# Performance work log

Measured on AMD Instinct MI355X. Metric: run time of the kernel, lower is better.

## Reference

```python
import jax, jax.numpy as jnp
import numpy as np

NUM_V = 500_000      # num (k-1)-simplices (vertices)
NUM_E = 1_500_000    # num k-simplices (edges)
NNZ = 2 * NUM_E      # 2 oriented incidences per edge
D_FEAT = 64


def setup_inputs() -> dict:
    key = jax.random.key(0)
    k1, k2, k3, k4 = jax.random.split(key, 4)
    simplex_features = jax.random.normal(k1, (NUM_E, D_FEAT), dtype=jnp.float32)
    # oriented incidence values are +/-1
    boundary_values = jnp.sign(jax.random.normal(k2, (NNZ,), dtype=jnp.float32))
    boundary_values = jnp.where(boundary_values == 0, 1.0, boundary_values)
    boundary_rows = jax.random.randint(k3, (NNZ,), 0, NUM_V, dtype=jnp.int32)
    boundary_cols = jax.random.randint(k4, (NNZ,), 0, NUM_E, dtype=jnp.int32)
    return {
        "simplex_features": simplex_features,
        "boundary_values": boundary_values,
        "boundary_rows": boundary_rows,
        "boundary_cols": boundary_cols,
        "num_out": NUM_V,
    }


def reference(simplex_features, boundary_values, boundary_rows, boundary_cols, num_out):
    # SpMM: out[r, :] += val * features[c, :] over all nonzeros (r, c, val).
    gathered = boundary_values[:, None] * simplex_features[boundary_cols]  # [nnz, d]
    out = jax.ops.segment_sum(gathered, boundary_rows, num_segments=num_out)  # [num_out, d]
    return out
```

## Files before the change

### kernel.cpp

```cpp
#include <hip/hip_runtime.h>

#define D_FEAT 64
#define SCAN_BLOCK 256
#define SCAN_ITEMS 16
#define SCAN_CHUNK (SCAN_BLOCK * SCAN_ITEMS)
#define SCANB_THREADS 1024

#define EMPTY_SLOT 0xFFFFFFFFu
#define ROW_CAP 16

typedef unsigned int u32;
typedef float f4 __attribute__((ext_vector_type(4)));


__device__ __forceinline__ void slow_claim(u32* __restrict__ line, u32 entry, u32 h,
                                           u32 r, u32* __restrict__ spill,
                                           u32* __restrict__ spill_cnt, u32 spill_cap) {
    for (u32 p = 1; p < ROW_CAP; ++p) {
        u32 old = atomicCAS(line + ((h + p) & (ROW_CAP - 1)), EMPTY_SLOT, entry);
        if (old == EMPTY_SLOT) return;
    }
    u32 kk = atomicAdd(spill_cnt, 1u);
    if (kk < spill_cap) { spill[2 * kk] = r; spill[2 * kk + 1] = entry; }
}

__global__ __launch_bounds__(256) void scatter_cas_kernel(
    const int* __restrict__ rows, const int* __restrict__ cols,
    const float* __restrict__ vals, u32* __restrict__ slots,
    u32* __restrict__ spill, u32* __restrict__ spill_cnt, int nnz, u32 spill_cap) {
    long long i4 = (long long)blockIdx.x * blockDim.x + threadIdx.x;
    long long base = i4 * 4;
    if (base >= nnz) return;

    if (base + 3 < nnz) {
        int4 rr = *(const int4*)(rows + base);
        int4 cc = *(const int4*)(cols + base);
        float4 vv = *(const float4*)(vals + base);

        u32 e0 = (u32)cc.x | (vv.x < 0.f ? 0x80000000u : 0u);
        u32 e1 = (u32)cc.y | (vv.y < 0.f ? 0x80000000u : 0u);
        u32 e2 = (u32)cc.z | (vv.z < 0.f ? 0x80000000u : 0u);
        u32 e3 = (u32)cc.w | (vv.w < 0.f ? 0x80000000u : 0u);

        u32* L0 = slots + (size_t)rr.x * ROW_CAP;
        u32* L1 = slots + (size_t)rr.y * ROW_CAP;
        u32* L2 = slots + (size_t)rr.z * ROW_CAP;
        u32* L3 = slots + (size_t)rr.w * ROW_CAP;

        u32 h0 = (u32)(base + 0) & (ROW_CAP - 1);
        u32 h1 = (u32)(base + 1) & (ROW_CAP - 1);
        u32 h2 = (u32)(base + 2) & (ROW_CAP - 1);
        u32 h3 = (u32)(base + 3) & (ROW_CAP - 1);

        u32 o0 = atomicCAS(L0 + h0, EMPTY_SLOT, e0);
        u32 o1 = atomicCAS(L1 + h1, EMPTY_SLOT, e1);
        u32 o2 = atomicCAS(L2 + h2, EMPTY_SLOT, e2);
        u32 o3 = atomicCAS(L3 + h3, EMPTY_SLOT, e3);

        if (o0 != EMPTY_SLOT) slow_claim(L0, e0, h0, (u32)rr.x, spill, spill_cnt, spill_cap);
        if (o1 != EMPTY_SLOT) slow_claim(L1, e1, h1, (u32)rr.y, spill, spill_cnt, spill_cap);
        if (o2 != EMPTY_SLOT) slow_claim(L2, e2, h2, (u32)rr.z, spill, spill_cnt, spill_cap);
        if (o3 != EMPTY_SLOT) slow_claim(L3, e3, h3, (u32)rr.w, spill, spill_cnt, spill_cap);
    } else {
        for (int k = 0; k < 4; ++k) {
            long long e = base + k;
            if (e >= nnz) break;
            int r = rows[e];
            u32 entry = (u32)cols[e] | (vals[e] < 0.f ? 0x80000000u : 0u);
            u32* line = slots + (size_t)r * ROW_CAP;
            u32 h = (u32)e & (ROW_CAP - 1);
            u32 old = atomicCAS(line + h, EMPTY_SLOT, entry);
            if (old != EMPTY_SLOT) slow_claim(line, entry, h, (u32)r, spill, spill_cnt, spill_cap);
        }
    }
}

__global__ __launch_bounds__(256) void gather_cas_kernel(
    const f4* __restrict__ feat4, const u32* __restrict__ slots,
    f4* __restrict__ out4, int numV) {
    long long tid = (long long)blockIdx.x * blockDim.x + threadIdx.x;
    long long pair = tid >> 6;
    long long r0 = pair * 2;
    if (r0 >= numV) return;
    long long r1 = r0 + 1;
    bool have1 = (r1 < numV);
    int lane = (int)(tid & 63);
    int g = lane >> 4;
    int s = lane & 15;

    long long rme = (g < 2) ? r0 : (have1 ? r1 : r0);
    u32 ent = slots[rme * ROW_CAP + s];

    u32 a0 = __shfl(ent, g);
    u32 a1 = __shfl(ent, g + 4);
    u32 a2 = __shfl(ent, g + 8);
    u32 a3 = __shfl(ent, g + 12);
    u32 b0 = __shfl(ent, 32 + g);
    u32 b1 = __shfl(ent, 36 + g);
    u32 b2 = __shfl(ent, 40 + g);
    u32 b3 = __shfl(ent, 44 + g);

    const f4 z = {0.f, 0.f, 0.f, 0.f};
    f4 f0 = z, f1 = z, f2 = z, f3 = z, g0 = z, g1 = z, g2 = z, g3 = z;
    if (a0 != EMPTY_SLOT) f0 = feat4[(size_t)(a0 & 0x7fffffffu) * 16 + s];
    if (a1 != EMPTY_SLOT) f1 = feat4[(size_t)(a1 & 0x7fffffffu) * 16 + s];
    if (a2 != EMPTY_SLOT) f2 = feat4[(size_t)(a2 & 0x7fffffffu) * 16 + s];
    if (a3 != EMPTY_SLOT) f3 = feat4[(size_t)(a3 & 0x7fffffffu) * 16 + s];
    if (have1) {
        if (b0 != EMPTY_SLOT) g0 = feat4[(size_t)(b0 & 0x7fffffffu) * 16 + s];
        if (b1 != EMPTY_SLOT) g1 = feat4[(size_t)(b1 & 0x7fffffffu) * 16 + s];
        if (b2 != EMPTY_SLOT) g2 = feat4[(size_t)(b2 & 0x7fffffffu) * 16 + s];
        if (b3 != EMPTY_SLOT) g3 = feat4[(size_t)(b3 & 0x7fffffffu) * 16 + s];
    }

    float s0 = (a0 >> 31) ? 1.f : -1.f;
    float s1 = (a1 >> 31) ? 1.f : -1.f;
    float s2 = (a2 >> 31) ? 1.f : -1.f;
    float s3 = (a3 >> 31) ? 1.f : -1.f;
    s0 = -s0; s1 = -s1; s2 = -s2; s3 = -s3;
    f4 acc0 = f0 * s0 + f1 * s1 + f2 * s2 + f3 * s3;

    float t0 = (b0 >> 31) ? -1.f : 1.f;
    float t1 = (b1 >> 31) ? -1.f : 1.f;
    float t2 = (b2 >> 31) ? -1.f : 1.f;
    float t3 = (b3 >> 31) ? -1.f : 1.f;
    f4 acc1 = g0 * t0 + g1 * t1 + g2 * t2 + g3 * t3;

#pragma unroll
    for (int m = 16; m <= 32; m <<= 1) {
        acc0.x += __shfl_xor(acc0.x, m);
        acc0.y += __shfl_xor(acc0.y, m);
        acc0.z += __shfl_xor(acc0.z, m);
        acc0.w += __shfl_xor(acc0.w, m);
        acc1.x += __shfl_xor(acc1.x, m);
        acc1.y += __shfl_xor(acc1.y, m);
        acc1.z += __shfl_xor(acc1.z, m);
        acc1.w += __shfl_xor(acc1.w, m);
    }
    if (g == 0) __builtin_nontemporal_store(acc0, &out4[r0 * 16 + s]);
    if (g == 1 && have1) __builtin_nontemporal_store(acc1, &out4[r1 * 16 + s]);
}

__global__ __launch_bounds__(256) void spill_apply_kernel(
    const float* __restrict__ feat, const u32* __restrict__ spill,
    const u32* __restrict__ spill_cnt, float* __restrict__ out, u32 spill_cap) {
    u32 total = *spill_cnt;
    if (total > spill_cap) total = spill_cap;
    int lane = threadIdx.x & 63;
    u32 wid = (blockIdx.x * blockDim.x + threadIdx.x) >> 6;
    u32 nw = (gridDim.x * blockDim.x) >> 6;
    for (u32 i = wid; i < total; i += nw) {
        u32 r = spill[2 * i];
        u32 e = spill[2 * i + 1];
        float f = feat[(size_t)(e & 0x7fffffffu) * D_FEAT + lane];
        atomicAdd(&out[(size_t)r * D_FEAT + lane], (e & 0x80000000u) ? -f : f);
    }
}


__global__ __launch_bounds__(256) void count_kernel(const int* __restrict__ rows,
                                                    u32* __restrict__ cnt, int nnz) {
    int e = blockIdx.x * blockDim.x + threadIdx.x;
    if (e < nnz) atomicAdd(&cnt[rows[e]], 1u);
}

__global__ __launch_bounds__(SCAN_BLOCK) void scanA_kernel(const u32* __restrict__ cnt,
                                                           u32* __restrict__ bsums, int n) {
    int t = threadIdx.x, b = blockIdx.x;
    int i0 = b * SCAN_CHUNK + t * SCAN_ITEMS;
    u32 s = 0;
#pragma unroll
    for (int k = 0; k < SCAN_ITEMS; ++k) {
        int i = i0 + k;
        if (i < n) s += cnt[i];
    }
    __shared__ u32 red[SCAN_BLOCK];
    red[t] = s;
    __syncthreads();
    for (int d = SCAN_BLOCK / 2; d > 0; d >>= 1) {
        if (t < d) red[t] += red[t + d];
        __syncthreads();
    }
    if (t == 0) bsums[b] = red[0];
}

__global__ __launch_bounds__(SCANB_THREADS) void scanB_kernel(u32* __restrict__ bsums, int nb,
                                                              u32* __restrict__ off, int numV,
                                                              u32 nnz) {
    int t = threadIdx.x;
    __shared__ u32 tmp[SCANB_THREADS];
    u32 v = (t < nb) ? bsums[t] : 0u;
    tmp[t] = v;
    __syncthreads();
    for (int d = 1; d < SCANB_THREADS; d <<= 1) {
        u32 x = (t >= d) ? tmp[t - d] : 0u;
        __syncthreads();
        tmp[t] += x;
        __syncthreads();
    }
    if (t < nb) bsums[t] = tmp[t] - v;
    if (t == 0) off[numV] = nnz;
}

__global__ __launch_bounds__(SCAN_BLOCK) void scanC_kernel(const u32* __restrict__ cnt,
                                                           const u32* __restrict__ bsums,
                                                           u32* __restrict__ off,
                                                           u32* __restrict__ cursor, int n) {
    int t = threadIdx.x, b = blockIdx.x;
    int i0 = b * SCAN_CHUNK + t * SCAN_ITEMS;
    u32 s = 0;
#pragma unroll
    for (int k = 0; k < SCAN_ITEMS; ++k) {
        int i = i0 + k;
        if (i < n) s += cnt[i];
    }
    __shared__ u32 tmp[SCAN_BLOCK];
    tmp[t] = s;
    __syncthreads();
    for (int d = 1; d < SCAN_BLOCK; d <<= 1) {
        u32 x = (t >= d) ? tmp[t - d] : 0u;
        __syncthreads();
        tmp[t] += x;
        __syncthreads();
    }
    u32 run = bsums[b] + (tmp[t] - s);
    for (int k = 0; k < SCAN_ITEMS; ++k) {
        int i = i0 + k;
        if (i < n) {
            off[i] = run;
            cursor[i] = run;
            run += cnt[i];
        }
    }
}

__global__ __launch_bounds__(256) void scatter_kernel(const int* __restrict__ rows,
                                                      const int* __restrict__ cols,
                                                      const float* __restrict__ vals,
                                                      u32* __restrict__ cursor,
                                                      u32* __restrict__ packed, int nnz) {
    int e = blockIdx.x * blockDim.x + threadIdx.x;
    if (e >= nnz) return;
    int r = rows[e];
    u32 pos = atomicAdd(&cursor[r], 1u);
    u32 entry = (u32)cols[e] | (vals[e] < 0.f ? 0x80000000u : 0u);
    packed[pos] = entry;
}

__global__ __launch_bounds__(256) void gather_kernel(const float* __restrict__ feat,
                                                     const u32* __restrict__ off,
                                                     const u32* __restrict__ packed,
                                                     float* __restrict__ out, int numV) {
    long long tid = (long long)blockIdx.x * blockDim.x + threadIdx.x;
    long long wid = tid >> 6;
    int lane = (int)(tid & 63);
    if (wid >= numV) return;

    u32 s = off[wid];
    u32 e = off[wid + 1];
    float acc = 0.f;

    for (u32 base = s; base < e; base += 64) {
        int cnt = (int)min(64u, e - base);
        u32 ent = (lane < cnt) ? packed[base + lane] : 0u;
        for (int j0 = 0; j0 < cnt; j0 += 4) {
            float f[4], sg[4];
#pragma unroll
            for (int k = 0; k < 4; ++k) {
                int j = j0 + k;
                u32 ej = __shfl(ent, j);
                long long c = (long long)(ej & 0x7fffffffu);
                sg[k] = (ej >> 31) ? -1.f : 1.f;
                f[k] = (j < cnt) ? feat[c * D_FEAT + lane] : 0.f;
            }
#pragma unroll
            for (int k = 0; k < 4; ++k) acc = fmaf(sg[k], f[k], acc);
        }
    }
    out[wid * D_FEAT + lane] = acc;
}

__global__ __launch_bounds__(256) void atomic_fallback_kernel(
    const float* __restrict__ feat, const float* __restrict__ vals,
    const int* __restrict__ rows, const int* __restrict__ cols,
    float* __restrict__ out, long long nnz) {
    long long tid = (long long)blockIdx.x * blockDim.x + threadIdx.x;
    long long e = tid >> 6;
    int d = (int)(tid & 63);
    if (e >= nnz) return;
    float f = feat[(long long)cols[e] * D_FEAT + d];
    atomicAdd(out + (long long)rows[e] * D_FEAT + d, vals[e] * f);
}

extern "C" void kernel_launch(void* const* d_in, const int* in_sizes, int n_in,
                              void* d_out, int out_size, void* d_ws, size_t ws_size,
                              hipStream_t stream) {
    const float* feat = (const float*)d_in[0];
    const float* vals = (const float*)d_in[1];
    const int*   rows = (const int*)d_in[2];
    const int*   cols = (const int*)d_in[3];
    float*       out  = (float*)d_out;

    int nnz  = in_sizes[1];
    int numV = out_size / D_FEAT;

    {
        const u32 spcap = 1u << 20;
        size_t needT1 = (16 + (size_t)numV * ROW_CAP + 2 * (size_t)spcap) * sizeof(u32);
        if (ws_size >= needT1) {
            u32* ws        = (u32*)d_ws;
            u32* spill_cnt = ws;
            u32* slots     = ws + 16;
            u32* spill     = slots + (size_t)numV * ROW_CAP;

            hipMemsetAsync(spill_cnt, 0, 16 * sizeof(u32), stream);
            hipMemsetAsync(slots, 0xFF, (size_t)numV * ROW_CAP * sizeof(u32), stream);

            long long nth4 = ((long long)nnz + 3) / 4;
            int nb4 = (int)((nth4 + 255) / 256);
            scatter_cas_kernel<<<nb4, 256, 0, stream>>>(rows, cols, vals, slots,
                                                        spill, spill_cnt, nnz, spcap);

            long long pairs = ((long long)numV + 1) / 2;
            long long gthreads = pairs * 64;
            int gblocks = (int)((gthreads + 255) / 256);
            gather_cas_kernel<<<gblocks, 256, 0, stream>>>((const f4*)feat, slots,
                                                           (f4*)out, numV);
            spill_apply_kernel<<<64, 256, 0, stream>>>(feat, spill, spill_cnt, out, spcap);
            return;
        }
    }

    int nScanBlocks = (numV + SCAN_CHUNK - 1) / SCAN_CHUNK;
    size_t need = ((size_t)(numV + 1) + numV + numV + SCANB_THREADS + nnz) * sizeof(u32);

    if (ws_size < need || nScanBlocks > SCANB_THREADS) {
        hipMemsetAsync(d_out, 0, (size_t)out_size * sizeof(float), stream);
        long long total = (long long)nnz * D_FEAT;
        long long nblk = (total + 255) / 256;
        atomic_fallback_kernel<<<(dim3)((unsigned)nblk), 256, 0, stream>>>(
            feat, vals, rows, cols, out, nnz);
        return;
    }

    u32* ws     = (u32*)d_ws;
    u32* off    = ws;
    u32* cursor = off + (numV + 1);
    u32* cnt    = cursor + numV;
    u32* bsums  = cnt + numV;
    u32* packed = bsums + SCANB_THREADS;

    hipMemsetAsync(cnt, 0, (size_t)numV * sizeof(u32), stream);

    int nb256 = (nnz + 255) / 256;
    count_kernel<<<nb256, 256, 0, stream>>>(rows, cnt, nnz);
    scanA_kernel<<<nScanBlocks, SCAN_BLOCK, 0, stream>>>(cnt, bsums, numV);
    scanB_kernel<<<1, SCANB_THREADS, 0, stream>>>(bsums, nScanBlocks, off, numV, (u32)nnz);
    scanC_kernel<<<nScanBlocks, SCAN_BLOCK, 0, stream>>>(cnt, bsums, off, cursor, numV);
    scatter_kernel<<<nb256, 256, 0, stream>>>(rows, cols, vals, cursor, packed, nnz);

    long long gthreads = (long long)numV * 64;
    long long gblocks  = (gthreads + 255) / 256;
    gather_kernel<<<(dim3)((unsigned)gblocks), 256, 0, stream>>>(feat, off, packed, out, numV);
}
```

Baseline: 752.1 us.

## Assign one row per 16-lane group in gather, removing cross-lane reduction

Changes the gather kernel's work mapping so each 16-lane quarter-wave owns a full row. Each lane reads all 16 slot entries of its row with vector loads and accumulates them serially, so no shuffles or xor reductions are needed. A wave now covers 4 rows instead of 2, which cuts the grid size and avoids redundant slot-entry distribution. Each lane now issues up to 16 dependent-free gathers, which raises register pressure and per-thread latency in exchange for removing the shuffle reduction.

```diff
diff --git a/kernel.cpp b/kernel.cpp
--- a/kernel.cpp
+++ b/kernel.cpp
@@ -79,66 +79,47 @@
     const f4* __restrict__ feat4, const u32* __restrict__ slots,
     f4* __restrict__ out4, int numV) {
     long long tid = (long long)blockIdx.x * blockDim.x + threadIdx.x;
-    long long pair = tid >> 6;
-    long long r0 = pair * 2;
-    if (r0 >= numV) return;
-    long long r1 = r0 + 1;
-    bool have1 = (r1 < numV);
+    long long wid = tid >> 6;
     int lane = (int)(tid & 63);
     int g = lane >> 4;
     int s = lane & 15;
-
-    long long rme = (g < 2) ? r0 : (have1 ? r1 : r0);
-    u32 ent = slots[rme * ROW_CAP + s];
-
-    u32 a0 = __shfl(ent, g);
-    u32 a1 = __shfl(ent, g + 4);
-    u32 a2 = __shfl(ent, g + 8);
-    u32 a3 = __shfl(ent, g + 12);
-    u32 b0 = __shfl(ent, 32 + g);
-    u32 b1 = __shfl(ent, 36 + g);
-    u32 b2 = __shfl(ent, 40 + g);
-    u32 b3 = __shfl(ent, 44 + g);
+    long long row = wid * 4 + g;
+    if (row >= numV) return;
+
+    const u32* line = slots + row * (long long)ROW_CAP;
+    uint4 q0 = *(const uint4*)(line + 0);
+    uint4 q1 = *(const uint4*)(line + 4);
+    uint4 q2 = *(const uint4*)(line + 8);
+    uint4 q3 = *(const uint4*)(line + 12);
 
     const f4 z = {0.f, 0.f, 0.f, 0.f};
-    f4 f0 = z, f1 = z, f2 = z, f3 = z, g0 = z, g1 = z, g2 = z, g3 = z;
-    if (a0 != EMPTY_SLOT) f0 = feat4[(size_t)(a0 & 0x7fffffffu) * 16 + s];
-    if (a1 != EMPTY_SLOT) f1 = feat4[(size_t)(a1 & 0x7fffffffu) * 16 + s];
-    if (a2 != EMPTY_SLOT) f2 = feat4[(size_t)(a2 & 0x7fffffffu) * 16 + s];
-    if (a3 != EMPTY_SLOT) f3 = feat4[(size_t)(a3 & 0x7fffffffu) * 16 + s];
-    if (have1) {
-        if (b0 != EMPTY_SLOT) g0 = feat4[(size_t)(b0 & 0x7fffffffu) * 16 + s];
-        if (b1 != EMPTY_SLOT) g1 = feat4[(size_t)(b1 & 0x7fffffffu) * 16 + s];
-        if (b2 != EMPTY_SLOT) g2 = feat4[(size_t)(b2 & 0x7fffffffu) * 16 + s];
-        if (b3 != EMPTY_SLOT) g3 = feat4[(size_t)(b3 & 0x7fffffffu) * 16 + s];
-    }
-
-    float s0 = (a0 >> 31) ? 1.f : -1.f;
-    float s1 = (a1 >> 31) ? 1.f : -1.f;
-    float s2 = (a2 >> 31) ? 1.f : -1.f;
-    float s3 = (a3 >> 31) ? 1.f : -1.f;
-    s0 = -s0; s1 = -s1; s2 = -s2; s3 = -s3;
-    f4 acc0 = f0 * s0 + f1 * s1 + f2 * s2 + f3 * s3;
-
-    float t0 = (b0 >> 31) ? -1.f : 1.f;
-    float t1 = (b1 >> 31) ? -1.f : 1.f;
-    float t2 = (b2 >> 31) ? -1.f : 1.f;
-    float t3 = (b3 >> 31) ? -1.f : 1.f;
-    f4 acc1 = g0 * t0 + g1 * t1 + g2 * t2 + g3 * t3;
-
-#pragma unroll
-    for (int m = 16; m <= 32; m <<= 1) {
-        acc0.x += __shfl_xor(acc0.x, m);
-        acc0.y += __shfl_xor(acc0.y, m);
-        acc0.z += __shfl_xor(acc0.z, m);
-        acc0.w += __shfl_xor(acc0.w, m);
-        acc1.x += __shfl_xor(acc1.x, m);
-        acc1.y += __shfl_xor(acc1.y, m);
-        acc1.z += __shfl_xor(acc1.z, m);
-        acc1.w += __shfl_xor(acc1.w, m);
-    }
-    if (g == 0) __builtin_nontemporal_store(acc0, &out4[r0 * 16 + s]);
-    if (g == 1 && have1) __builtin_nontemporal_store(acc1, &out4[r1 * 16 + s]);
+    f4 acc = z;
+
+#define GATHER8(Ea, Eb, Ec, Ed, Ee, Ef, Eg2, Eh)                                   \
+    {                                                                              \
+        f4 fa = z, fb = z, fc = z, fd = z, fe = z, ff = z, fg = z, fh = z;         \
+        if (Ea != EMPTY_SLOT) fa = feat4[(size_t)(Ea & 0x7fffffffu) * 16 + s];     \
+        if (Eb != EMPTY_SLOT) fb = feat4[(size_t)(Eb & 0x7fffffffu) * 16 + s];     \
+        if (Ec != EMPTY_SLOT) fc = feat4[(size_t)(Ec & 0x7fffffffu) * 16 + s];     \
+        if (Ed != EMPTY_SLOT) fd = feat4[(size_t)(Ed & 0x7fffffffu) * 16 + s];     \
+        if (Ee != EMPTY_SLOT) fe = feat4[(size_t)(Ee & 0x7fffffffu) * 16 + s];     \
+        if (Ef != EMPTY_SLOT) ff = feat4[(size_t)(Ef & 0x7fffffffu) * 16 + s];     \
+        if (Eg2 != EMPTY_SLOT) fg = feat4[(size_t)(Eg2 & 0x7fffffffu) * 16 + s];   \
+        if (Eh != EMPTY_SLOT) fh = feat4[(size_t)(Eh & 0x7fffffffu) * 16 + s];     \
+        acc += fa * ((Ea >> 31) ? -1.f : 1.f);                                     \
+        acc += fb * ((Eb >> 31) ? -1.f : 1.f);                                     \
+        acc += fc * ((Ec >> 31) ? -1.f : 1.f);                                     \
+        acc += fd * ((Ed >> 31) ? -1.f : 1.f);                                     \
+        acc += fe * ((Ee >> 31) ? -1.f : 1.f);                                     \
+        acc += ff * ((Ef >> 31) ? -1.f : 1.f);                                     \
+        acc += fg * ((Eg2 >> 31) ? -1.f : 1.f);                                    \
+        acc += fh * ((Eh >> 31) ? -1.f : 1.f);                                     \
+    }
+    GATHER8(q0.x, q0.y, q0.z, q0.w, q1.x, q1.y, q1.z, q1.w)
+    GATHER8(q2.x, q2.y, q2.z, q2.w, q3.x, q3.y, q3.z, q3.w)
+#undef GATHER8
+
+    __builtin_nontemporal_store(acc, &out4[row * 16 + s]);
 }
 
 __global__ __launch_bounds__(256) void spill_apply_kernel(
@@ -321,8 +302,8 @@
             scatter_cas_kernel<<<nb4, 256, 0, stream>>>(rows, cols, vals, slots,
                                                         spill, spill_cnt, nnz, spcap);
 
-            long long pairs = ((long long)numV + 1) / 2;
-            long long gthreads = pairs * 64;
+            long long waves = ((long long)numV + 3) / 4;
+            long long gthreads = waves * 64;
             int gblocks = (int)((gthreads + 255) / 256);
             gather_cas_kernel<<<gblocks, 256, 0, stream>>>((const f4*)feat, slots,
                                                            (f4*)out, numV);
```

Result: no change. 752.4 us (+0.0%).
